# Optimization experiments

Hardware: AMD Instinct MI355X
Metric: run time of the kernel (lower is better)

Reference implementation:

```python
import jax, jax.numpy as jnp
import numpy as np

B = 1
NUM_STAGES = 3
HIDDEN_LENGTH = (512, 1024, 1536)
TOTAL = sum(HIDDEN_LENGTH)
ENC = 128
DIM = 1536
HEADS = 24
HEAD_DIM = 64
INNER = 4 * DIM
EPS = 1e-6
SCALE = HEAD_DIM ** -0.5


def _rope_freqs(S):
    # rotation-matrix RoPE table: [S, 1, D/2, 2, 2]
    pos = np.arange(S, dtype=np.float64)
    inv = 1.0 / (10000.0 ** (np.arange(0, HEAD_DIM, 2, dtype=np.float64) / HEAD_DIM))
    ang = pos[:, None] * inv[None, :]
    cos, sin = np.cos(ang), np.sin(ang)
    rot = np.stack([np.stack([cos, -sin], -1), np.stack([sin, cos], -1)], -2)
    return jnp.asarray(rot[:, None], dtype=jnp.float32)


def _layer_norm(x):
    m = x.mean(-1, keepdims=True)
    v = ((x - m) ** 2).mean(-1, keepdims=True)
    return (x - m) * jax.lax.rsqrt(v + EPS)


def _rms_norm(x, w):
    v = (x ** 2).mean(-1, keepdims=True)
    return x * jax.lax.rsqrt(v + EPS) * w


def _apply_rope(x, rot):
    # x: [B, S, H, D]; rot: [S, 1, D/2, 2, 2]
    xr = x.reshape(x.shape[:-1] + (HEAD_DIM // 2, 1, 2))
    out = rot[..., 0] * xr[..., 0] + rot[..., 1] * xr[..., 1]  # [B,S,H,D/2,2]
    return out.reshape(x.shape)


def _adaln_tokens(e6):
    # e6: [B*NUM_STAGES, 6*DIM] -> ragged per-token broadcast [B, TOTAL, 6*DIM]
    segs = [jnp.broadcast_to(e6[i::NUM_STAGES][:, None, :], (B, L, e6.shape[-1]))
            for i, L in enumerate(HIDDEN_LENGTH)]
    return jnp.concatenate(segs, axis=1)


def _ff(x, w1, b1, w2, b2):
    return jnp.dot(jax.nn.gelu(jnp.dot(x, w1) + b1, approximate=True), w2) + b2


def _forward(hidden_states, encoder_hidden_states, temb, enc_valid, rope_0, rope_1, rope_2,
             ada_w, ada_b, ada_ctx_w, ada_ctx_b,
             wq, bq, wk, bk, wv, bv, waq, baq, wak, bak, wav, bav,
             nq_w, nk_w, naq_w, nak_w, wo, bo, wao, bao,
             ff_w1, ff_b1, ff_w2, ff_b2, ffc_w1, ffc_b1, ffc_w2, ffc_b2):
    ropes = (rope_0, rope_1, rope_2)
    # AdaLN-Zero on hidden tokens (ragged per-stage modulation)
    tok = _adaln_tokens(jnp.dot(jax.nn.silu(temb), ada_w) + ada_b)
    shift_msa, scale_msa, gate_msa, shift_mlp, scale_mlp, gate_mlp = jnp.split(tok, 6, axis=2)
    nh = _layer_norm(hidden_states) * (1 + scale_msa) + shift_msa
    # AdaLN-Zero on context tokens
    ec = jnp.dot(jax.nn.silu(temb), ada_ctx_w) + ada_ctx_b
    c_shift, c_scale, c_gate, c_shift_mlp, c_scale_mlp, c_gate_mlp = jnp.split(ec, 6, axis=1)
    ne = _layer_norm(encoder_hidden_states) * (1 + c_scale[:, None]) + c_shift[:, None]

    # QKV projections + per-head RMSNorm on q/k
    q = _rms_norm((nh @ wq + bq).reshape(B, TOTAL, HEADS, HEAD_DIM), nq_w)
    k = _rms_norm((nh @ wk + bk).reshape(B, TOTAL, HEADS, HEAD_DIM), nk_w)
    v = (nh @ wv + bv).reshape(B, TOTAL, HEADS, HEAD_DIM)
    eq = _rms_norm((ne @ waq + baq).reshape(B * NUM_STAGES, ENC, HEADS, HEAD_DIM), naq_w)
    ek = _rms_norm((ne @ wak + bak).reshape(B * NUM_STAGES, ENC, HEADS, HEAD_DIM), nak_w)
    ev = (ne @ wav + bav).reshape(B * NUM_STAGES, ENC, HEADS, HEAD_DIM)

    hid_out, enc_out = [], []
    i_sum = 0
    for i, L in enumerate(HIDDEN_LENGTH):
        qi = _apply_rope(jnp.concatenate([eq[i::NUM_STAGES], q[:, i_sum:i_sum + L]], 1), ropes[i])
        ki = _apply_rope(jnp.concatenate([ek[i::NUM_STAGES], k[:, i_sum:i_sum + L]], 1), ropes[i])
        vi = jnp.concatenate([ev[i::NUM_STAGES], v[:, i_sum:i_sum + L]], 1)
        # T5-style key mask: only first enc_valid[i,b] text tokens are valid keys
        key_ok = jnp.concatenate([jnp.arange(ENC)[None, :] < enc_valid[i][:, None],
                                  jnp.ones((B, L), bool)], 1)  # [B, ENC+L]
        s = jnp.einsum('bqhd,bkhd->bhqk', qi, ki) * SCALE
        s = jnp.where(key_ok[:, None, None, :], s, jnp.finfo(s.dtype).min)
        o = jnp.einsum('bhqk,bkhd->bqhd', jax.nn.softmax(s, -1), vi).reshape(B, ENC + L, DIM)
        enc_out.append(o[:, :ENC])
        hid_out.append(o[:, ENC:])
        i_sum += L
    attn_h = jnp.concatenate(hid_out, 1) @ wo + bo
    attn_e = jnp.stack(enc_out, 1).reshape(B * NUM_STAGES, ENC, DIM) @ wao + bao

    # gated residuals + FFN
    h = hidden_states + gate_msa * attn_h
    h = h + gate_mlp * _ff(_layer_norm(h) * (1 + scale_mlp) + shift_mlp, ff_w1, ff_b1, ff_w2, ff_b2)
    e = encoder_hidden_states + c_gate[:, None] * attn_e
    e = e + c_gate_mlp[:, None] * _ff(_layer_norm(e) * (1 + c_scale_mlp[:, None]) + c_shift_mlp[:, None],
                                      ffc_w1, ffc_b1, ffc_w2, ffc_b2)
    return e, h


def setup_inputs() -> dict:
    ks = iter(jax.random.split(jax.random.key(0), 48))

    def nrm(shape, s):
        return jax.random.normal(next(ks), shape, jnp.float32) * s

    Z = lambda *shape: jnp.zeros(shape, jnp.float32)
    O = lambda *shape: jnp.ones(shape, jnp.float32)
    inp = {
        'hidden_states': nrm((B, TOTAL, DIM), 1.0),
        'encoder_hidden_states': nrm((B * NUM_STAGES, ENC, DIM), 1.0),
        'temb': nrm((B * NUM_STAGES, DIM), 1.0),
        'enc_valid': jax.random.randint(next(ks), (NUM_STAGES, B), 64, ENC + 1),
        'rope_0': _rope_freqs(ENC + HIDDEN_LENGTH[0]),
        'rope_1': _rope_freqs(ENC + HIDDEN_LENGTH[1]),
        'rope_2': _rope_freqs(ENC + HIDDEN_LENGTH[2]),
        'ada_w': nrm((DIM, 6 * DIM), 0.02), 'ada_b': nrm((6 * DIM,), 0.02),
        'ada_ctx_w': nrm((DIM, 6 * DIM), 0.02), 'ada_ctx_b': nrm((6 * DIM,), 0.02),
        'wq': nrm((DIM, DIM), 0.02), 'bq': Z(DIM),
        'wk': nrm((DIM, DIM), 0.02), 'bk': Z(DIM),
        'wv': nrm((DIM, DIM), 0.02), 'bv': Z(DIM),
        'waq': nrm((DIM, DIM), 0.02), 'baq': Z(DIM),
        'wak': nrm((DIM, DIM), 0.02), 'bak': Z(DIM),
        'wav': nrm((DIM, DIM), 0.02), 'bav': Z(DIM),
        'nq_w': O(HEAD_DIM), 'nk_w': O(HEAD_DIM), 'naq_w': O(HEAD_DIM), 'nak_w': O(HEAD_DIM),
        'wo': nrm((DIM, DIM), 0.02), 'bo': Z(DIM),
        'wao': nrm((DIM, DIM), 0.02), 'bao': Z(DIM),
        'ff_w1': nrm((DIM, INNER), 0.02), 'ff_b1': Z(INNER),
        'ff_w2': nrm((INNER, DIM), 0.02), 'ff_b2': Z(DIM),
        'ffc_w1': nrm((DIM, INNER), 0.02), 'ffc_b1': Z(INNER),
        'ffc_w2': nrm((INNER, DIM), 0.02), 'ffc_b2': Z(DIM),
    }
    return inp


def reference(hidden_states, encoder_hidden_states, temb, enc_valid, rope_0, rope_1, rope_2,
              ada_w, ada_b, ada_ctx_w, ada_ctx_b,
              wq, bq, wk, bk, wv, bv, waq, baq, wak, bak, wav, bav,
              nq_w, nk_w, naq_w, nak_w, wo, bo, wao, bao,
              ff_w1, ff_b1, ff_w2, ff_b2, ffc_w1, ffc_b1, ffc_w2, ffc_b2):
    return _forward(hidden_states, encoder_hidden_states, temb, enc_valid, rope_0, rope_1, rope_2,
                    ada_w, ada_b, ada_ctx_w, ada_ctx_b,
                    wq, bq, wk, bk, wv, bv, waq, baq, wak, bak, wav, bav,
                    nq_w, nk_w, naq_w, nak_w, wo, bo, wao, bao,
                    ff_w1, ff_b1, ff_w2, ff_b2, ffc_w1, ffc_b1, ffc_w2, ffc_b2)
```

## Files before the change

### kernel.cpp

```cpp
#include <hip/hip_runtime.h>
#include <hip/hip_bf16.h>

typedef __hip_bfloat16 bf16;
typedef short s16x8 __attribute__((ext_vector_type(8)));
typedef float f32x4 __attribute__((ext_vector_type(4)));

#define DIM   1536
#define HEADS 24
#define HD    64
#define TOTAL 3072
#define ENCR  384
#define INNER 6144
#define SIX   9216

__device__ __forceinline__ float ldf(const void* p, size_t i, int f) {
    return f ? ((const float*)p)[i]
             : __bfloat162float(((const bf16*)p)[i]);
}
__device__ __forceinline__ short f2s(float v) {
    bf16 b = __float2bfloat16(v);
    short s; __builtin_memcpy(&s, &b, 2); return s;
}
__device__ __forceinline__ s16x8 ldb8(const void* B, size_t i, int f) {
    s16x8 r;
    if (f) {
        const float4* p = (const float4*)((const float*)B + i);
        float4 x = p[0], y = p[1];
        r[0]=f2s(x.x); r[1]=f2s(x.y); r[2]=f2s(x.z); r[3]=f2s(x.w);
        r[4]=f2s(y.x); r[5]=f2s(y.y); r[6]=f2s(y.z); r[7]=f2s(y.w);
    } else {
        r = *(const s16x8*)((const short*)B + i);
    }
    return r;
}
__device__ __forceinline__ void gld16(const void* g, void* l) {
    __builtin_amdgcn_global_load_lds(
        (const __attribute__((address_space(1))) unsigned int*)g,
        (__attribute__((address_space(3))) unsigned int*)l, 16, 0, 0);
}

__global__ __launch_bounds__(256) void probe_kernel(const unsigned short* __restrict__ w,
                                                    int* __restrict__ flag) {
    __shared__ int cnt;
    if (threadIdx.x == 0) cnt = 0;
    __syncthreads();
    int local = 0;
    for (int i = threadIdx.x; i < 65536; i += 256) {
        unsigned short u = w[i];
        if (((u >> 7) & 0xFF) == 0xFF) local++;
    }
    atomicAdd(&cnt, local);
    __syncthreads();
    if (threadIdx.x == 0) flag[0] = (cnt > 0) ? 1 : 0;
}

__global__ __launch_bounds__(256) void silu_kernel(const void* __restrict__ temb,
                                                   float* __restrict__ sact,
                                                   const int* __restrict__ flag) {
    int f = flag[0];
    int i = blockIdx.x * 256 + threadIdx.x;
    float x = ldf(temb, i, f);
    sact[i] = x / (1.f + __expf(-x));
}

__global__ __launch_bounds__(256) void ada_kernel(const float* __restrict__ sact,
                                                  const void* __restrict__ W1,
                                                  const void* __restrict__ b1,
                                                  float* __restrict__ o1,
                                                  const void* __restrict__ W2,
                                                  const void* __restrict__ b2,
                                                  float* __restrict__ o2,
                                                  const int* __restrict__ flag) {
    int f = flag[0];
    __shared__ float red[3][4][64];
    int bx = blockIdx.x;
    const void* W; const void* bias; float* out;
    if (bx < 144) { W = W1; bias = b1; out = o1; }
    else          { W = W2; bias = b2; out = o2; bx -= 144; }
    int c   = threadIdx.x & 63;
    int col = bx * 64 + c;
    int kq  = threadIdx.x >> 6;
    float a0 = 0.f, a1 = 0.f, a2 = 0.f;
    for (int k = kq * 384; k < kq * 384 + 384; ++k) {
        float wv = ldf(W, (size_t)k * SIX + col, f);
        a0 += sact[k] * wv;
        a1 += sact[1536 + k] * wv;
        a2 += sact[3072 + k] * wv;
    }
    red[0][kq][c] = a0; red[1][kq][c] = a1; red[2][kq][c] = a2;
    __syncthreads();
    if (kq < 3) {
        float s = red[kq][0][c] + red[kq][1][c] + red[kq][2][c] + red[kq][3][c]
                + ldf(bias, col, f);
        out[(size_t)kq * SIX + col] = s;
    }
}

__global__ __launch_bounds__(256) void ln_mod_kernel(const void* __restrict__ xh,
                                                     const void* __restrict__ xe,
                                                     const float* __restrict__ adaH,
                                                     const float* __restrict__ adaE,
                                                     bf16* __restrict__ outh,
                                                     bf16* __restrict__ oute,
                                                     const int* __restrict__ flag) {
    int f = flag[0];
    __shared__ float r1[256], r2[256];
    int t = blockIdx.x, tid = threadIdx.x;
    const void* x; bf16* out; const float* ada; int stage;
    if (t < TOTAL) { x = xh; out = outh; ada = adaH; stage = t < 512 ? 0 : (t < 1536 ? 1 : 2); }
    else           { t -= TOTAL; x = xe; out = oute; ada = adaE; stage = t >> 7; }
    float v[6]; float s = 0.f, s2 = 0.f;
#pragma unroll
    for (int i = 0; i < 6; ++i) {
        float a = ldf(x, (size_t)t * DIM + tid + i * 256, f);
        v[i] = a; s += a; s2 += a * a;
    }
    r1[tid] = s; r2[tid] = s2;
    __syncthreads();
    for (int st = 128; st; st >>= 1) {
        if (tid < st) { r1[tid] += r1[tid + st]; r2[tid] += r2[tid + st]; }
        __syncthreads();
    }
    float mean = r1[0] * (1.f / 1536.f);
    float var  = fmaxf(r2[0] * (1.f / 1536.f) - mean * mean, 0.f);
    float inv  = rsqrtf(var + 1e-6f);
    const float* ab = ada + (size_t)stage * SIX;
#pragma unroll
    for (int i = 0; i < 6; ++i) {
        int c = tid + i * 256;
        float sc = ab[1 * DIM + c];
        float sh = ab[0 * DIM + c];
        out[(size_t)t * DIM + c] = __float2bfloat16((v[i] - mean) * inv * (1.f + sc) + sh);
    }
}

__global__ __launch_bounds__(256) void resid_ln_kernel(const void* __restrict__ bh,
                                                       const bf16* __restrict__ dh,
                                                       const float* __restrict__ adaH,
                                                       bf16* __restrict__ resh,
                                                       bf16* __restrict__ outh,
                                                       const void* __restrict__ be,
                                                       const bf16* __restrict__ de,
                                                       const float* __restrict__ adaE,
                                                       bf16* __restrict__ rese,
                                                       bf16* __restrict__ oute,
                                                       const int* __restrict__ flag) {
    int f = flag[0];
    __shared__ float r1[256], r2[256];
    int t = blockIdx.x, tid = threadIdx.x;
    const void* base; const bf16* delta; const float* ada; bf16* res; bf16* out; int stage;
    if (t < TOTAL) { base = bh; delta = dh; ada = adaH; res = resh; out = outh;
                     stage = t < 512 ? 0 : (t < 1536 ? 1 : 2); }
    else           { t -= TOTAL; base = be; delta = de; ada = adaE; res = rese; out = oute;
                     stage = t >> 7; }
    const float* ab = ada + (size_t)stage * SIX;
    float v[6]; float s = 0.f, s2 = 0.f;
#pragma unroll
    for (int i = 0; i < 6; ++i) {
        int c = tid + i * 256;
        size_t gi = (size_t)t * DIM + c;
        float g = ab[2 * DIM + c];
        float a = ldf(base, gi, f) + g * __bfloat162float(delta[gi]);
        res[gi] = __float2bfloat16(a);
        v[i] = a; s += a; s2 += a * a;
    }
    r1[tid] = s; r2[tid] = s2;
    __syncthreads();
    for (int st = 128; st; st >>= 1) {
        if (tid < st) { r1[tid] += r1[tid + st]; r2[tid] += r2[tid + st]; }
        __syncthreads();
    }
    float mean = r1[0] * (1.f / 1536.f);
    float var  = fmaxf(r2[0] * (1.f / 1536.f) - mean * mean, 0.f);
    float inv  = rsqrtf(var + 1e-6f);
#pragma unroll
    for (int i = 0; i < 6; ++i) {
        int c = tid + i * 256;
        float sc = ab[4 * DIM + c];
        float sh = ab[3 * DIM + c];
        out[(size_t)t * DIM + c] = __float2bfloat16((v[i] - mean) * inv * (1.f + sc) + sh);
    }
}

__device__ __forceinline__ void wt_body(const void* W, bf16* WT, int K, int N, int f) {
    __shared__ short T[64][72];
    int n0 = blockIdx.x * 64, k0 = blockIdx.y * 64;
    int tid = threadIdx.x;
    int r = tid >> 2, c0 = (tid & 3) * 16;
#pragma unroll
    for (int i = 0; i < 16; ++i)
        T[r][c0 + i] = f2s(ldf(W, (size_t)(k0 + r) * N + n0 + c0 + i, f));
    __syncthreads();
    int n = tid >> 2, kc = (tid & 3) * 16;
    s16x8 o0, o1;
#pragma unroll
    for (int i = 0; i < 8; ++i) o0[i] = T[kc + i][n];
#pragma unroll
    for (int i = 0; i < 8; ++i) o1[i] = T[kc + 8 + i][n];
    short* orow = (short*)WT + (size_t)(n0 + n) * K + k0 + kc;
    *(s16x8*)orow = o0;
    *(s16x8*)(orow + 8) = o1;
}

__global__ __launch_bounds__(256) void wt8_kernel(const void* s0, const void* s1,
                                                  const void* s2, const void* s3,
                                                  const void* s4, const void* s5,
                                                  const void* s6, const void* s7,
                                                  bf16* d0, bf16* d1, bf16* d2, bf16* d3,
                                                  bf16* d4, bf16* d5, bf16* d6, bf16* d7,
                                                  const int* __restrict__ flag) {
    const void* W; bf16* WT;
    switch (blockIdx.z) {
        case 0: W = s0; WT = d0; break;  case 1: W = s1; WT = d1; break;
        case 2: W = s2; WT = d2; break;  case 3: W = s3; WT = d3; break;
        case 4: W = s4; WT = d4; break;  case 5: W = s5; WT = d5; break;
        case 6: W = s6; WT = d6; break;  default: W = s7; WT = d7; break;
    }
    wt_body(W, WT, DIM, DIM, flag[0]);
}

__global__ __launch_bounds__(256) void wt2_kernel(const void* s0, const void* s1,
                                                  bf16* d0, bf16* d1, int K, int N,
                                                  const int* __restrict__ flag) {
    const void* W = blockIdx.z ? s1 : s0;
    bf16* WT = blockIdx.z ? d1 : d0;
    wt_body(W, WT, K, N, flag[0]);
}

__global__ __launch_bounds__(256) void gemm_t_kernel(const short* __restrict__ Ah,
                                                     const short* __restrict__ Ae,
                                                     const short* __restrict__ Bth,
                                                     const short* __restrict__ Bte,
                                                     const void* Bh0, const void* Bh1, const void* Bh2,
                                                     const void* Be0, const void* Be1, const void* Be2,
                                                     bf16* Oh0, bf16* Oh1, bf16* Oh2,
                                                     bf16* Oe0, bf16* Oe1, bf16* Oe2,
                                                     int yh, int Nout, int K, int act,
                                                     const int* __restrict__ flag) {
    int f = flag[0];
    __shared__ __align__(16) short As0[128 * 32];
    __shared__ __align__(16) short As1[128 * 32];
    __shared__ __align__(16) short As2[128 * 32];
    __shared__ __align__(16) short Bs0[128 * 32];
    __shared__ __align__(16) short Bs1[128 * 32];
    __shared__ __align__(16) short Bs2[128 * 32];
    int tid = threadIdx.x;
    int lane = tid & 63, wid = tid >> 6;
    int wy = wid >> 1, wx = wid & 1;
    int lane15 = lane & 15, quad = lane >> 4;

    int gx = gridDim.x;
    int nwg = gx * gridDim.y;
    int orig = blockIdx.y * gx + blockIdx.x;
    int q = nwg >> 3, r = nwg & 7;
    int x8 = orig & 7, o8 = orig >> 3;
    int wg = (x8 < r) ? x8 * (q + 1) + o8 : r * (q + 1) + (x8 - r) * q + o8;
    int bx = wg % gx, by = wg / gx;

    const short* A; const short* Bt; int m0;
    const void *b0, *b1, *b2; bf16 *o0, *o1, *o2;
    if (by < yh) { A = Ah; Bt = Bth; m0 = by * 128;
                   b0 = Bh0; b1 = Bh1; b2 = Bh2; o0 = Oh0; o1 = Oh1; o2 = Oh2; }
    else         { A = Ae; Bt = Bte; m0 = (by - yh) * 128;
                   b0 = Be0; b1 = Be1; b2 = Be2; o0 = Oe0; o1 = Oe1; o2 = Oe2; }
    int n0 = bx * 128;
    int lr = lane >> 2, lc = lane & 3;

    f32x4 acc[4][4] = {};

    auto stage = [&](short* Ad, short* Bd, int k0) {
#pragma unroll
        for (int c = 0; c < 2; ++c) {
            int rb = wid * 32 + c * 16;
            int rr = rb + lr;
            int gc = (lc - (rr >> 1)) & 3;
            gld16(A  + (size_t)(m0 + rr) * K + k0 + gc * 8, Ad + rb * 32);
            gld16(Bt + (size_t)(n0 + rr) * K + k0 + gc * 8, Bd + rb * 32);
        }
    };
    auto compute = [&](const short* Ash, const short* Bsh) {
        s16x8 af[4], bfr[4];
#pragma unroll
        for (int i = 0; i < 4; ++i) {
            int ra = wy * 64 + i * 16 + lane15;
            af[i] = *(const s16x8*)&Ash[ra * 32 + ((quad + (ra >> 1)) & 3) * 8];
            int rb2 = wx * 64 + i * 16 + lane15;
            bfr[i] = *(const s16x8*)&Bsh[rb2 * 32 + ((quad + (rb2 >> 1)) & 3) * 8];
        }
#pragma unroll
        for (int im = 0; im < 4; ++im)
#pragma unroll
            for (int in = 0; in < 4; ++in)
                acc[im][in] = __builtin_amdgcn_mfma_f32_16x16x32_bf16(
                    af[im], bfr[in], acc[im][in], 0, 0, 0);
    };
    int nt = K >> 5;
    auto step = [&](const short* Ac, const short* Bc, short* An, short* Bn, int tt) {
        int nx = tt + 2;
        if (nx < nt) {
            stage(An, Bn, nx << 5);
            asm volatile("s_waitcnt vmcnt(8)" ::: "memory");
        } else if (tt + 1 < nt) {
            asm volatile("s_waitcnt vmcnt(4)" ::: "memory");
        } else {
            asm volatile("s_waitcnt vmcnt(0)" ::: "memory");
        }
        __builtin_amdgcn_s_barrier();
        compute(Ac, Bc);
        asm volatile("s_waitcnt lgkmcnt(0)" ::: "memory");
        __builtin_amdgcn_s_barrier();
    };

    stage(As0, Bs0, 0);
    stage(As1, Bs1, 32);
    for (int t = 0; t < nt; t += 3) {
        step(As0, Bs0, As2, Bs2, t);
        step(As1, Bs1, As0, Bs0, t + 1);
        step(As2, Bs2, As1, Bs1, t + 2);
    }

    int sel = n0 / Nout;
    int nb = n0 - sel * Nout;
    bf16* Cout = sel == 0 ? o0 : (sel == 1 ? o1 : o2);
    const void* bs = sel == 0 ? b0 : (sel == 1 ? b1 : b2);

#pragma unroll
    for (int in = 0; in < 4; ++in) {
        int gn = nb + wx * 64 + in * 16 + lane15;
        float bsv = ldf(bs, gn, f);
#pragma unroll
        for (int im = 0; im < 4; ++im) {
#pragma unroll
            for (int rr = 0; rr < 4; ++rr) {
                int gm = m0 + wy * 64 + im * 16 + quad * 4 + rr;
                float v = acc[im][in][rr] + bsv;
                if (act == 1) {
                    float u = 0.7978845608028654f * (v + 0.044715f * v * v * v);
                    float e = __expf(2.f * u);
                    v = 0.5f * v * (1.f + (1.f - 2.f / (e + 1.f)));
                }
                Cout[(size_t)gm * Nout + gn] = __float2bfloat16(v);
            }
        }
    }
}

#define LDK 48
__global__ __launch_bounds__(256) void gemm_kernel(const short* __restrict__ A,
                                                   const void* __restrict__ B,
                                                   const void* __restrict__ bias,
                                                   bf16* __restrict__ C,
                                                   int M, int N, int K, int act,
                                                   const int* __restrict__ flag) {
    int f = flag[0];
    __shared__ __align__(16) short As[128 * LDK];
    __shared__ __align__(16) short Bs[128 * LDK];
    int tid = threadIdx.x;
    int lane = tid & 63, wid = tid >> 6;
    int wy = wid >> 1, wx = wid & 1;
    int m16 = lane & 15, quad = lane >> 4;
    int m0 = blockIdx.y * 128, n0 = blockIdx.x * 128;
    int ar0 = tid >> 2;
    int ac  = (tid & 3) * 8;
    int br0 = tid >> 4;
    int bc  = (tid & 15) * 8;
    f32x4 acc[4][4] = {};
    for (int k0 = 0; k0 < K; k0 += 32) {
        s16x8 a0 = *(const s16x8*)(A + (size_t)(m0 + ar0) * K + k0 + ac);
        s16x8 a1 = *(const s16x8*)(A + (size_t)(m0 + ar0 + 64) * K + k0 + ac);
        s16x8 b0 = ldb8(B, (size_t)(k0 + br0) * N + n0 + bc, f);
        s16x8 b1 = ldb8(B, (size_t)(k0 + br0 + 16) * N + n0 + bc, f);
        __syncthreads();
        *(s16x8*)(&As[ar0 * LDK + ac]) = a0;
        *(s16x8*)(&As[(ar0 + 64) * LDK + ac]) = a1;
#pragma unroll
        for (int i = 0; i < 8; ++i) {
            Bs[(bc + i) * LDK + br0] = b0[i];
            Bs[(bc + i) * LDK + br0 + 16] = b1[i];
        }
        __syncthreads();
        s16x8 af[4], bfr[4];
#pragma unroll
        for (int i = 0; i < 4; ++i) {
            af[i]  = *(const s16x8*)(&As[(wy * 64 + i * 16 + m16) * LDK + quad * 8]);
            bfr[i] = *(const s16x8*)(&Bs[(wx * 64 + i * 16 + m16) * LDK + quad * 8]);
        }
#pragma unroll
        for (int im = 0; im < 4; ++im)
#pragma unroll
            for (int in = 0; in < 4; ++in)
                acc[im][in] = __builtin_amdgcn_mfma_f32_16x16x32_bf16(
                    af[im], bfr[in], acc[im][in], 0, 0, 0);
    }
#pragma unroll
    for (int in = 0; in < 4; ++in) {
        int gn = n0 + wx * 64 + in * 16 + m16;
        float bsv = ldf(bias, gn, f);
#pragma unroll
        for (int im = 0; im < 4; ++im) {
#pragma unroll
            for (int r = 0; r < 4; ++r) {
                int gm = m0 + wy * 64 + im * 16 + quad * 4 + r;
                float v = acc[im][in][r] + bsv;
                if (act == 1) {
                    float u = 0.7978845608028654f * (v + 0.044715f * v * v * v);
                    float e = __expf(2.f * u);
                    v = 0.5f * v * (1.f + (1.f - 2.f / (e + 1.f)));
                }
                C[(size_t)gm * N + gn] = __float2bfloat16(v);
            }
        }
    }
}

__global__ __launch_bounds__(256) void rmsrope_kernel(bf16* __restrict__ Qb,
                                                      bf16* __restrict__ Kb,
                                                      bf16* __restrict__ EQb,
                                                      bf16* __restrict__ EKb,
                                                      const void* __restrict__ nq,
                                                      const void* __restrict__ nk,
                                                      const void* __restrict__ naq,
                                                      const void* __restrict__ nak,
                                                      const void* __restrict__ r0,
                                                      const void* __restrict__ r1,
                                                      const void* __restrict__ r2,
                                                      const int* __restrict__ flag) {
    int f = flag[0];
    int bid = blockIdx.x;
    bf16* x; const void* w; int is_enc;
    if (bid < 9216)       { x = Qb;  w = nq;  is_enc = 0; }
    else if (bid < 18432) { x = Kb;  w = nk;  is_enc = 0; bid -= 9216; }
    else if (bid < 19584) { x = EQb; w = naq; is_enc = 1; bid -= 18432; }
    else                  { x = EKb; w = nak; is_enc = 1; bid -= 19584; }
    int grp = bid * 8 + (threadIdx.x >> 5);
    int l = threadIdx.x & 31;
    int t = grp / 24;
    size_t base = (size_t)grp * 64 + 2 * l;
    unsigned int u = *(const unsigned int*)((const short*)x + base);
    union { unsigned int ui; float fl; } a, b;
    a.ui = (u & 0xFFFFu) << 16;
    b.ui = u & 0xFFFF0000u;
    float x0 = a.fl, x1 = b.fl;
    float ss = x0 * x0 + x1 * x1;
#pragma unroll
    for (int off = 1; off < 32; off <<= 1) ss += __shfl_xor(ss, off);
    float inv = rsqrtf(ss * (1.f / 64.f) + 1e-6f);
    float xw0 = x0 * inv * ldf(w, 2 * l, f);
    float xw1 = x1 * inv * ldf(w, 2 * l + 1, f);
    int stage, pos;
    if (is_enc)        { stage = t >> 7; pos = t & 127; }
    else if (t < 512)  { stage = 0; pos = 128 + t; }
    else if (t < 1536) { stage = 1; pos = 128 + t - 512; }
    else               { stage = 2; pos = 128 + t - 1536; }
    const void* rt = stage == 0 ? r0 : (stage == 1 ? r1 : r2);
    size_t ro = ((size_t)pos * 32 + l) * 4;
    float c00 = ldf(rt, ro + 0, f);
    float c01 = ldf(rt, ro + 1, f);
    float c10 = ldf(rt, ro + 2, f);
    float c11 = ldf(rt, ro + 3, f);
    unsigned int q0 = (unsigned int)(unsigned short)f2s(c00 * xw0 + c01 * xw1);
    unsigned int q1 = (unsigned int)(unsigned short)f2s(c10 * xw0 + c11 * xw1);
    *(unsigned int*)((short*)x + base) = (q1 << 16) | q0;
}

__global__ __launch_bounds__(256) void vjt_kernel(const bf16* __restrict__ Vb,
                                                  const bf16* __restrict__ EVb,
                                                  bf16* __restrict__ VJt) {
    __shared__ short T[64][72];
    int b = blockIdx.x;
    int h = b % 24, jt = b / 24;
    int s, j0, S, hbase; size_t off;
    if (jt < 10)      { s = 0; j0 = jt * 64;        S = 640;  hbase = 0;    off = 0; }
    else if (jt < 28) { s = 1; j0 = (jt - 10) * 64; S = 1152; hbase = 512;  off = (size_t)24 * 64 * 640; }
    else              { s = 2; j0 = (jt - 28) * 64; S = 1664; hbase = 1536; off = (size_t)24 * 64 * (640 + 1152); }
    int tid = threadIdx.x;
    int tr = tid >> 2, tc = (tid & 3) * 16;
    int j = j0 + tr;
    const bf16* vr = (j < 128) ? EVb + ((size_t)(s * 128 + j) * DIM + h * HD)
                               : Vb + ((size_t)(hbase + j - 128) * DIM + h * HD);
    *(s16x8*)&T[tr][tc]     = *(const s16x8*)((const short*)vr + tc);
    *(s16x8*)&T[tr][tc + 8] = *(const s16x8*)((const short*)vr + tc + 8);
    __syncthreads();
    int d = tid >> 2, c0 = (tid & 3) * 16;
    s16x8 o0, o1;
#pragma unroll
    for (int i = 0; i < 8; ++i) o0[i] = T[c0 + i][d];
#pragma unroll
    for (int i = 0; i < 8; ++i) o1[i] = T[c0 + 8 + i][d];
    short* orow = (short*)VJt + off + (size_t)(h * HD + d) * S + j0 + c0;
    *(s16x8*)orow = o0;
    *(s16x8*)(orow + 8) = o1;
}

__global__ __launch_bounds__(256) void attn_mfma_kernel(const bf16* __restrict__ Qb,
                                                        const bf16* __restrict__ Kb,
                                                        const bf16* __restrict__ EQ,
                                                        const bf16* __restrict__ EK,
                                                        const bf16* __restrict__ VJt,
                                                        const int* __restrict__ encv,
                                                        bf16* __restrict__ AH,
                                                        bf16* __restrict__ AE) {
    __shared__ __align__(16) short Ks[64 * 72];
    __shared__ __align__(16) short Vt[64 * 72];
    __shared__ __align__(16) short Ps[4][16 * 72];
    int tid = threadIdx.x, wid = tid >> 6, lane = tid & 63;
    int lane15 = lane & 15, quad = lane >> 4;
    int b = (int)gridDim.x - 1 - (int)blockIdx.x;
    int h = b % 24, qt = b / 24;
    int s, qt0, S, hbase; size_t voff;
    if (qt < 10)      { s = 0; qt0 = qt;      S = 640;  hbase = 0;    voff = 0; }
    else if (qt < 28) { s = 1; qt0 = qt - 10; S = 1152; hbase = 512;  voff = (size_t)24 * 64 * 640; }
    else              { s = 2; qt0 = qt - 28; S = 1664; hbase = 1536; voff = (size_t)24 * 64 * (640 + 1152); }
    const short* vbase = (const short*)VJt + voff + (size_t)h * HD * S;
    int ev = encv[s];
    int qbase = qt0 * 64 + wid * 16;

    int q = qbase + lane15;
    const short* qrow = (q < 128)
        ? (const short*)EQ + ((size_t)(s * 128 + q) * DIM + h * HD)
        : (const short*)Qb + ((size_t)(hbase + q - 128) * DIM + h * HD);
    s16x8 qa[2];
#pragma unroll
    for (int k0 = 0; k0 < 2; ++k0) {
        s16x8 x = *(const s16x8*)(qrow + k0 * 32 + quad * 8);
#pragma unroll
        for (int i = 0; i < 8; ++i) {
            union { unsigned int u; float fl; } t;
            t.u = ((unsigned int)(unsigned short)x[i]) << 16;
            t.fl *= 0.125f;
            x[i] = (short)(t.u >> 16);
        }
        qa[k0] = x;
    }

    f32x4 o[4] = {};
    float mrun[4] = {-1e30f, -1e30f, -1e30f, -1e30f};
    float lrun[4] = {};

    int nkb = S >> 6;
    for (int kb = 0; kb < nkb; ++kb) {
        __syncthreads();
        {
            int kr = tid >> 2, kc = (tid & 3) * 16;
            int kg = kb * 64 + kr;
            const short* krow = (kg < 128)
                ? (const short*)EK + ((size_t)(s * 128 + kg) * DIM + h * HD)
                : (const short*)Kb + ((size_t)(hbase + kg - 128) * DIM + h * HD);
            *(s16x8*)&Ks[kr * 72 + kc]     = *(const s16x8*)(krow + kc);
            *(s16x8*)&Ks[kr * 72 + kc + 8] = *(const s16x8*)(krow + kc + 8);
        }
        {
            int vd = tid >> 2, vc = (tid & 3) * 16;
            const short* vrow = vbase + (size_t)vd * S + kb * 64 + vc;
            *(s16x8*)&Vt[vd * 72 + vc]     = *(const s16x8*)(vrow);
            *(s16x8*)&Vt[vd * 72 + vc + 8] = *(const s16x8*)(vrow + 8);
        }
        __syncthreads();

        f32x4 sacc[4];
        __builtin_amdgcn_s_setprio(1);
#pragma unroll
        for (int g = 0; g < 4; ++g) {
            s16x8 kf0 = *(const s16x8*)&Ks[(g * 16 + lane15) * 72 + quad * 8];
            s16x8 kf1 = *(const s16x8*)&Ks[(g * 16 + lane15) * 72 + 32 + quad * 8];
            f32x4 c = {};
            c = __builtin_amdgcn_mfma_f32_16x16x32_bf16(qa[0], kf0, c, 0, 0, 0);
            c = __builtin_amdgcn_mfma_f32_16x16x32_bf16(qa[1], kf1, c, 0, 0, 0);
            sacc[g] = c;
        }
        __builtin_amdgcn_s_setprio(0);
        if (kb == 1) {
#pragma unroll
            for (int g = 0; g < 4; ++g) {
                int keyg = 64 + g * 16 + lane15;
                if (keyg >= ev) {
#pragma unroll
                    for (int r = 0; r < 4; ++r) sacc[g][r] = -1e30f;
                }
            }
        }
        float mt[4], al[4], ps[4];
#pragma unroll
        for (int r = 0; r < 4; ++r)
            mt[r] = fmaxf(fmaxf(sacc[0][r], sacc[1][r]), fmaxf(sacc[2][r], sacc[3][r]));
#pragma unroll
        for (int off = 1; off < 16; off <<= 1)
#pragma unroll
            for (int r = 0; r < 4; ++r) mt[r] = fmaxf(mt[r], __shfl_xor(mt[r], off));
#pragma unroll
        for (int r = 0; r < 4; ++r) {
            float mn = fmaxf(mrun[r], mt[r]);
            al[r] = __expf(mrun[r] - mn);
            mrun[r] = mn;
        }
#pragma unroll
        for (int g = 0; g < 4; ++g)
#pragma unroll
            for (int r = 0; r < 4; ++r)
                sacc[g][r] = __expf(sacc[g][r] - mrun[r]);
#pragma unroll
        for (int r = 0; r < 4; ++r)
            ps[r] = (sacc[0][r] + sacc[1][r]) + (sacc[2][r] + sacc[3][r]);
#pragma unroll
        for (int off = 1; off < 16; off <<= 1)
#pragma unroll
            for (int r = 0; r < 4; ++r) ps[r] += __shfl_xor(ps[r], off);
#pragma unroll
        for (int r = 0; r < 4; ++r) lrun[r] = lrun[r] * al[r] + ps[r];
#pragma unroll
        for (int dc = 0; dc < 4; ++dc)
#pragma unroll
            for (int r = 0; r < 4; ++r) o[dc][r] *= al[r];
#pragma unroll
        for (int g = 0; g < 4; ++g)
#pragma unroll
            for (int r = 0; r < 4; ++r)
                Ps[wid][(quad * 4 + r) * 72 + g * 16 + lane15] = f2s(sacc[g][r]);
        s16x8 pa0 = *(const s16x8*)&Ps[wid][lane15 * 72 + quad * 8];
        s16x8 pa1 = *(const s16x8*)&Ps[wid][lane15 * 72 + 32 + quad * 8];
        __builtin_amdgcn_s_setprio(1);
#pragma unroll
        for (int dc = 0; dc < 4; ++dc) {
            s16x8 vf0 = *(const s16x8*)&Vt[(dc * 16 + lane15) * 72 + quad * 8];
            s16x8 vf1 = *(const s16x8*)&Vt[(dc * 16 + lane15) * 72 + 32 + quad * 8];
            o[dc] = __builtin_amdgcn_mfma_f32_16x16x32_bf16(pa0, vf0, o[dc], 0, 0, 0);
            o[dc] = __builtin_amdgcn_mfma_f32_16x16x32_bf16(pa1, vf1, o[dc], 0, 0, 0);
        }
        __builtin_amdgcn_s_setprio(0);
    }

    float invl[4];
#pragma unroll
    for (int r = 0; r < 4; ++r) invl[r] = 1.f / fmaxf(lrun[r], 1e-37f);
#pragma unroll
    for (int r = 0; r < 4; ++r) {
        int qr = qbase + quad * 4 + r;
        bf16* orow = (qr < 128)
            ? AE + ((size_t)(s * 128 + qr) * DIM + h * HD)
            : AH + ((size_t)(hbase + qr - 128) * DIM + h * HD);
#pragma unroll
        for (int dc = 0; dc < 4; ++dc)
            orow[dc * 16 + lane15] = __float2bfloat16(o[dc][r] * invl[r]);
    }
}

__global__ __launch_bounds__(256) void resid_out_kernel(const bf16* __restrict__ bh,
                                                        const bf16* __restrict__ dh,
                                                        const float* __restrict__ adaH,
                                                        const bf16* __restrict__ be,
                                                        const bf16* __restrict__ de,
                                                        const float* __restrict__ adaE,
                                                        void* __restrict__ out,
                                                        const int* __restrict__ flag) {
    int ofl = flag[0];
    int bid = blockIdx.x, tid = threadIdx.x;
    float v; size_t oidx;
    if (bid < 2304) {
        int gid = bid * 256 + tid;
        int t = gid / DIM, c = gid - t * DIM;
        int st = t >> 7;
        v = __bfloat162float(be[gid]) + adaE[(size_t)st * SIX + 5 * DIM + c] * __bfloat162float(de[gid]);
        oidx = gid;
    } else {
        int gid = (bid - 2304) * 256 + tid;
        int t = gid / DIM, c = gid - t * DIM;
        int st = t < 512 ? 0 : (t < 1536 ? 1 : 2);
        v = __bfloat162float(bh[gid]) + adaH[(size_t)st * SIX + 5 * DIM + c] * __bfloat162float(dh[gid]);
        oidx = (size_t)ENCR * DIM + gid;
    }
    if (ofl) ((float*)out)[oidx] = v;
    else     ((bf16*)out)[oidx] = __float2bfloat16(v);
}

extern "C" void kernel_launch(void* const* d_in, const int* in_sizes, int n_in,
                              void* d_out, int out_size, void* d_ws, size_t ws_size,
                              hipStream_t stream) {
    (void)in_sizes; (void)n_in; (void)out_size;
    const void* hid   = d_in[0];
    const void* enc   = d_in[1];
    const void* temb  = d_in[2];
    const int*  encv  = (const int*)d_in[3];
    const void* rope0 = d_in[4];
    const void* rope1 = d_in[5];
    const void* rope2 = d_in[6];
    const void* ada_w = d_in[7];  const void* ada_b = d_in[8];
    const void* ada_cw = d_in[9]; const void* ada_cb = d_in[10];
    const void* wq = d_in[11]; const void* bq = d_in[12];
    const void* wk = d_in[13]; const void* bk = d_in[14];
    const void* wv = d_in[15]; const void* bv = d_in[16];
    const void* waq = d_in[17]; const void* baq = d_in[18];
    const void* wak = d_in[19]; const void* bak = d_in[20];
    const void* wav = d_in[21]; const void* bav = d_in[22];
    const void* nq_w = d_in[23];
    const void* nk_w = d_in[24];
    const void* naq_w = d_in[25];
    const void* nak_w = d_in[26];
    const void* wo = d_in[27]; const void* bo = d_in[28];
    const void* wao = d_in[29]; const void* bao = d_in[30];
    const void* ffw1 = d_in[31]; const void* ffb1 = d_in[32];
    const void* ffw2 = d_in[33]; const void* ffb2 = d_in[34];
    const void* fcw1 = d_in[35]; const void* fcb1 = d_in[36];
    const void* fcw2 = d_in[37]; const void* fcb2 = d_in[38];

    char* ws = (char*)d_ws;
    size_t off = 0;
    auto alloc = [&](size_t bytes) {
        char* p = ws + off;
        off = (off + bytes + 255) & ~(size_t)255;
        return p;
    };
    int*   FLAG = (int*)alloc(256);
    float* SACT = (float*)alloc(3 * 1536 * 4);
    float* E6   = (float*)alloc((size_t)3 * SIX * 4);
    float* EC   = (float*)alloc((size_t)3 * SIX * 4);
    bf16* NH  = (bf16*)alloc((size_t)TOTAL * DIM * 2);
    bf16* NE  = (bf16*)alloc((size_t)ENCR * DIM * 2);
    bf16* Qb  = (bf16*)alloc((size_t)TOTAL * DIM * 2);
    bf16* Kb  = (bf16*)alloc((size_t)TOTAL * DIM * 2);
    bf16* Vb  = (bf16*)alloc((size_t)TOTAL * DIM * 2);
    bf16* EQb = (bf16*)alloc((size_t)ENCR * DIM * 2);
    bf16* EKb = (bf16*)alloc((size_t)ENCR * DIM * 2);
    bf16* EVb = (bf16*)alloc((size_t)ENCR * DIM * 2);
    bf16* VJT = (bf16*)alloc((size_t)24 * 64 * (640 + 1152 + 1664) * 2);
    bf16* FF1  = (bf16*)alloc((size_t)TOTAL * INNER * 2);
    bf16* FFC1 = (bf16*)alloc((size_t)ENCR * INNER * 2);
    const size_t SQ = (size_t)DIM * DIM;
    const size_t RC = (size_t)DIM * INNER;
    bf16* WQKVT  = (bf16*)alloc(3 * SQ * 2);
    bf16* WAQKVT = (bf16*)alloc(3 * SQ * 2);
    bf16* WOT    = (bf16*)alloc(SQ * 2);
    bf16* WAOT   = (bf16*)alloc(SQ * 2);
    bf16* FFW1T  = (bf16*)alloc(RC * 2);
    bf16* FFW2T  = (bf16*)alloc(RC * 2);
    bf16* FCW1T  = (bf16*)alloc(RC * 2);
    bf16* FCW2T  = (bf16*)alloc(RC * 2);
    bool useT = (off <= ws_size);

    probe_kernel<<<1, 256, 0, stream>>>((const unsigned short*)ada_w, FLAG);

    if (useT) {
        wt8_kernel<<<dim3(24, 24, 8), 256, 0, stream>>>(
            wq, wk, wv, waq, wak, wav, wo, wao,
            WQKVT, WQKVT + SQ, WQKVT + 2 * SQ,
            WAQKVT, WAQKVT + SQ, WAQKVT + 2 * SQ,
            WOT, WAOT, FLAG);
        wt2_kernel<<<dim3(96, 24, 2), 256, 0, stream>>>(ffw1, fcw1, FFW1T, FCW1T, DIM, INNER, FLAG);
        wt2_kernel<<<dim3(24, 96, 2), 256, 0, stream>>>(ffw2, fcw2, FFW2T, FCW2T, INNER, DIM, FLAG);
    }

    silu_kernel<<<18, 256, 0, stream>>>(temb, SACT, FLAG);
    ada_kernel<<<288, 256, 0, stream>>>(SACT, ada_w, ada_b, E6, ada_cw, ada_cb, EC, FLAG);

    ln_mod_kernel<<<TOTAL + ENCR, 256, 0, stream>>>(hid, enc, E6, EC, NH, NE, FLAG);

    if (useT) {
        gemm_t_kernel<<<dim3(36, 27), 256, 0, stream>>>(
            (const short*)NH, (const short*)NE, (const short*)WQKVT, (const short*)WAQKVT,
            bq, bk, bv, baq, bak, bav,
            Qb, Kb, Vb, EQb, EKb, EVb, 24, DIM, DIM, 0, FLAG);
    } else {
        dim3 gh(12, 24), ge(12, 3);
        gemm_kernel<<<gh, 256, 0, stream>>>((const short*)NH, wq, bq, Qb, TOTAL, DIM, DIM, 0, FLAG);
        gemm_kernel<<<gh, 256, 0, stream>>>((const short*)NH, wk, bk, Kb, TOTAL, DIM, DIM, 0, FLAG);
        gemm_kernel<<<gh, 256, 0, stream>>>((const short*)NH, wv, bv, Vb, TOTAL, DIM, DIM, 0, FLAG);
        gemm_kernel<<<ge, 256, 0, stream>>>((const short*)NE, waq, baq, EQb, ENCR, DIM, DIM, 0, FLAG);
        gemm_kernel<<<ge, 256, 0, stream>>>((const short*)NE, wak, bak, EKb, ENCR, DIM, DIM, 0, FLAG);
        gemm_kernel<<<ge, 256, 0, stream>>>((const short*)NE, wav, bav, EVb, ENCR, DIM, DIM, 0, FLAG);
    }

    rmsrope_kernel<<<20736, 256, 0, stream>>>(Qb, Kb, EQb, EKb,
                                              nq_w, nk_w, naq_w, nak_w,
                                              rope0, rope1, rope2, FLAG);

    vjt_kernel<<<1296, 256, 0, stream>>>(Vb, EVb, VJT);

    attn_mfma_kernel<<<1296, 256, 0, stream>>>(Qb, Kb, EQb, EKb, VJT, encv, NH, NE);

    if (useT) {
        gemm_t_kernel<<<dim3(12, 27), 256, 0, stream>>>(
            (const short*)NH, (const short*)NE, (const short*)WOT, (const short*)WAOT,
            bo, bo, bo, bao, bao, bao,
            Qb, Qb, Qb, EQb, EQb, EQb, 24, DIM, DIM, 0, FLAG);
    } else {
        dim3 gh(12, 24), ge(12, 3);
        gemm_kernel<<<gh, 256, 0, stream>>>((const short*)NH, wo, bo, Qb, TOTAL, DIM, DIM, 0, FLAG);
        gemm_kernel<<<ge, 256, 0, stream>>>((const short*)NE, wao, bao, EQb, ENCR, DIM, DIM, 0, FLAG);
    }

    resid_ln_kernel<<<TOTAL + ENCR, 256, 0, stream>>>(hid, Qb, E6, Kb, Vb,
                                                      enc, EQb, EC, EKb, EVb, FLAG);

    if (useT) {
        gemm_t_kernel<<<dim3(48, 27), 256, 0, stream>>>(
            (const short*)Vb, (const short*)EVb, (const short*)FFW1T, (const short*)FCW1T,
            ffb1, ffb1, ffb1, fcb1, fcb1, fcb1,
            FF1, FF1, FF1, FFC1, FFC1, FFC1, 24, INNER, DIM, 1, FLAG);
        gemm_t_kernel<<<dim3(12, 27), 256, 0, stream>>>(
            (const short*)FF1, (const short*)FFC1, (const short*)FFW2T, (const short*)FCW2T,
            ffb2, ffb2, ffb2, fcb2, fcb2, fcb2,
            NH, NH, NH, NE, NE, NE, 24, DIM, INNER, 0, FLAG);
    } else {
        dim3 gh(12, 24), ge(12, 3), gf1(48, 24), gf1e(48, 3);
        gemm_kernel<<<gf1, 256, 0, stream>>>((const short*)Vb, ffw1, ffb1, FF1, TOTAL, INNER, DIM, 1, FLAG);
        gemm_kernel<<<gf1e, 256, 0, stream>>>((const short*)EVb, fcw1, fcb1, FFC1, ENCR, INNER, DIM, 1, FLAG);
        gemm_kernel<<<gh, 256, 0, stream>>>((const short*)FF1, ffw2, ffb2, NH, TOTAL, DIM, INNER, 0, FLAG);
        gemm_kernel<<<ge, 256, 0, stream>>>((const short*)FFC1, fcw2, fcb2, NE, ENCR, DIM, INNER, 0, FLAG);
    }

    resid_out_kernel<<<20736, 256, 0, stream>>>(Kb, NH, E6, EKb, NE, EC, d_out, FLAG);
}
```

Before: 1.135 ms.

## Fuse prep kernels, vectorize transposes, deepen GEMM ring and merge rmsrope with V transpose

The weight-transpose, SiLU and AdaLN projection launches are merged into one prep_kernel. Each AdaLN block now recomputes the SiLU of temb into shared memory. The transpose body switches from scalar loads to 8-wide vector loads. The GEMM ring grows from three to four shared-memory buffers so the trailing lgkmcnt wait and second barrier per k-step can be dropped, at the cost of more LDS per block and possibly lower occupancy. The RMSNorm/RoPE kernel and the V-transpose kernel are merged into one launch to cut launch overhead and let the two workloads overlap.

```diff
diff --git a/kernel.cpp b/kernel.cpp
--- a/kernel.cpp
+++ b/kernel.cpp
@@ -54,32 +54,81 @@
     if (threadIdx.x == 0) flag[0] = (cnt > 0) ? 1 : 0;
 }
 
-__global__ __launch_bounds__(256) void silu_kernel(const void* __restrict__ temb,
-                                                   float* __restrict__ sact,
-                                                   const int* __restrict__ flag) {
+__device__ __forceinline__ void wt_body(const void* W, bf16* WT, int K, int N,
+                                        int n0, int k0, int f) {
+    __shared__ short T[64][72];
+    int tid = threadIdx.x;
+    int r = tid >> 2, c0 = (tid & 3) * 16;
+    s16x8 v0 = ldb8(W, (size_t)(k0 + r) * N + n0 + c0, f);
+    s16x8 v1 = ldb8(W, (size_t)(k0 + r) * N + n0 + c0 + 8, f);
+    *(s16x8*)&T[r][c0] = v0;
+    *(s16x8*)&T[r][c0 + 8] = v1;
+    __syncthreads();
+    int n = tid >> 2, kc = (tid & 3) * 16;
+    s16x8 o0, o1;
+#pragma unroll
+    for (int i = 0; i < 8; ++i) o0[i] = T[kc + i][n];
+#pragma unroll
+    for (int i = 0; i < 8; ++i) o1[i] = T[kc + 8 + i][n];
+    short* orow = (short*)WT + (size_t)(n0 + n) * K + k0 + kc;
+    *(s16x8*)orow = o0;
+    *(s16x8*)(orow + 8) = o1;
+}
+
+__global__ __launch_bounds__(256) void prep_kernel(
+        const void* wq, const void* wk, const void* wv,
+        const void* waq, const void* wak, const void* wav,
+        const void* wo, const void* wao,
+        bf16* dq0, bf16* dq1, bf16* dq2, bf16* dq3,
+        bf16* dq4, bf16* dq5, bf16* dq6, bf16* dq7,
+        const void* ffw1, const void* fcw1, bf16* FFW1T, bf16* FCW1T,
+        const void* ffw2, const void* fcw2, bf16* FFW2T, bf16* FCW2T,
+        const void* temb,
+        const void* adaW1, const void* adaB1, float* adaO1,
+        const void* adaW2, const void* adaB2, float* adaO2,
+        int do_wt, const int* __restrict__ flag) {
     int f = flag[0];
-    int i = blockIdx.x * 256 + threadIdx.x;
-    float x = ldf(temb, i, f);
-    sact[i] = x / (1.f + __expf(-x));
-}
-
-__global__ __launch_bounds__(256) void ada_kernel(const float* __restrict__ sact,
-                                                  const void* __restrict__ W1,
-                                                  const void* __restrict__ b1,
-                                                  float* __restrict__ o1,
-                                                  const void* __restrict__ W2,
-                                                  const void* __restrict__ b2,
-                                                  float* __restrict__ o2,
-                                                  const int* __restrict__ flag) {
-    int f = flag[0];
+    int bid = blockIdx.x;
+    if (bid < 13824) {
+        if (!do_wt) return;
+        if (bid < 4608) {
+            int m = bid / 576, w = bid % 576;
+            const void* W; bf16* WT;
+            switch (m) {
+                case 0: W = wq;  WT = dq0; break;  case 1: W = wk;  WT = dq1; break;
+                case 2: W = wv;  WT = dq2; break;  case 3: W = waq; WT = dq3; break;
+                case 4: W = wak; WT = dq4; break;  case 5: W = wav; WT = dq5; break;
+                case 6: W = wo;  WT = dq6; break;  default: W = wao; WT = dq7; break;
+            }
+            wt_body(W, WT, DIM, DIM, (w % 24) * 64, (w / 24) * 64, f);
+        } else if (bid < 9216) {
+            int r2 = bid - 4608;
+            int m = r2 / 2304, w = r2 % 2304;
+            wt_body(m ? fcw1 : ffw1, m ? FCW1T : FFW1T, DIM, INNER,
+                    (w % 96) * 64, (w / 96) * 64, f);
+        } else {
+            int r2 = bid - 9216;
+            int m = r2 / 2304, w = r2 % 2304;
+            wt_body(m ? fcw2 : ffw2, m ? FCW2T : FFW2T, INNER, DIM,
+                    (w % 24) * 64, (w / 24) * 64, f);
+        }
+        return;
+    }
+    __shared__ float sact[4608];
     __shared__ float red[3][4][64];
-    int bx = blockIdx.x;
+    int tid = threadIdx.x;
+    for (int i = tid; i < 4608; i += 256) {
+        float x = ldf(temb, i, f);
+        sact[i] = x / (1.f + __expf(-x));
+    }
+    __syncthreads();
+    int bx = bid - 13824;
     const void* W; const void* bias; float* out;
-    if (bx < 144) { W = W1; bias = b1; out = o1; }
-    else          { W = W2; bias = b2; out = o2; bx -= 144; }
-    int c   = threadIdx.x & 63;
+    if (bx < 144) { W = adaW1; bias = adaB1; out = adaO1; }
+    else          { W = adaW2; bias = adaB2; out = adaO2; bx -= 144; }
+    int c   = tid & 63;
     int col = bx * 64 + c;
-    int kq  = threadIdx.x >> 6;
+    int kq  = tid >> 6;
     float a0 = 0.f, a1 = 0.f, a2 = 0.f;
     for (int k = kq * 384; k < kq * 384 + 384; ++k) {
         float wv = ldf(W, (size_t)k * SIX + col, f);
@@ -182,51 +231,6 @@
     }
 }
 
-__device__ __forceinline__ void wt_body(const void* W, bf16* WT, int K, int N, int f) {
-    __shared__ short T[64][72];
-    int n0 = blockIdx.x * 64, k0 = blockIdx.y * 64;
-    int tid = threadIdx.x;
-    int r = tid >> 2, c0 = (tid & 3) * 16;
-#pragma unroll
-    for (int i = 0; i < 16; ++i)
-        T[r][c0 + i] = f2s(ldf(W, (size_t)(k0 + r) * N + n0 + c0 + i, f));
-    __syncthreads();
-    int n = tid >> 2, kc = (tid & 3) * 16;
-    s16x8 o0, o1;
-#pragma unroll
-    for (int i = 0; i < 8; ++i) o0[i] = T[kc + i][n];
-#pragma unroll
-    for (int i = 0; i < 8; ++i) o1[i] = T[kc + 8 + i][n];
-    short* orow = (short*)WT + (size_t)(n0 + n) * K + k0 + kc;
-    *(s16x8*)orow = o0;
-    *(s16x8*)(orow + 8) = o1;
-}
-
-__global__ __launch_bounds__(256) void wt8_kernel(const void* s0, const void* s1,
-                                                  const void* s2, const void* s3,
-                                                  const void* s4, const void* s5,
-                                                  const void* s6, const void* s7,
-                                                  bf16* d0, bf16* d1, bf16* d2, bf16* d3,
-                                                  bf16* d4, bf16* d5, bf16* d6, bf16* d7,
-                                                  const int* __restrict__ flag) {
-    const void* W; bf16* WT;
-    switch (blockIdx.z) {
-        case 0: W = s0; WT = d0; break;  case 1: W = s1; WT = d1; break;
-        case 2: W = s2; WT = d2; break;  case 3: W = s3; WT = d3; break;
-        case 4: W = s4; WT = d4; break;  case 5: W = s5; WT = d5; break;
-        case 6: W = s6; WT = d6; break;  default: W = s7; WT = d7; break;
-    }
-    wt_body(W, WT, DIM, DIM, flag[0]);
-}
-
-__global__ __launch_bounds__(256) void wt2_kernel(const void* s0, const void* s1,
-                                                  bf16* d0, bf16* d1, int K, int N,
-                                                  const int* __restrict__ flag) {
-    const void* W = blockIdx.z ? s1 : s0;
-    bf16* WT = blockIdx.z ? d1 : d0;
-    wt_body(W, WT, K, N, flag[0]);
-}
-
 __global__ __launch_bounds__(256) void gemm_t_kernel(const short* __restrict__ Ah,
                                                      const short* __restrict__ Ae,
                                                      const short* __restrict__ Bth,
@@ -241,9 +245,11 @@
     __shared__ __align__(16) short As0[128 * 32];
     __shared__ __align__(16) short As1[128 * 32];
     __shared__ __align__(16) short As2[128 * 32];
+    __shared__ __align__(16) short As3[128 * 32];
     __shared__ __align__(16) short Bs0[128 * 32];
     __shared__ __align__(16) short Bs1[128 * 32];
     __shared__ __align__(16) short Bs2[128 * 32];
+    __shared__ __align__(16) short Bs3[128 * 32];
     int tid = threadIdx.x;
     int lane = tid & 63, wid = tid >> 6;
     int wy = wid >> 1, wx = wid & 1;
@@ -306,17 +312,17 @@
             asm volatile("s_waitcnt vmcnt(0)" ::: "memory");
         }
         __builtin_amdgcn_s_barrier();
+        __builtin_amdgcn_sched_barrier(0);
         compute(Ac, Bc);
-        asm volatile("s_waitcnt lgkmcnt(0)" ::: "memory");
-        __builtin_amdgcn_s_barrier();
     };
 
     stage(As0, Bs0, 0);
     stage(As1, Bs1, 32);
-    for (int t = 0; t < nt; t += 3) {
+    for (int t = 0; t < nt; t += 4) {
         step(As0, Bs0, As2, Bs2, t);
-        step(As1, Bs1, As0, Bs0, t + 1);
-        step(As2, Bs2, As1, Bs1, t + 2);
+        step(As1, Bs1, As3, Bs3, t + 1);
+        step(As2, Bs2, As0, Bs0, t + 2);
+        step(As3, Bs3, As1, Bs1, t + 3);
     }
 
     int sel = n0 / Nout;
@@ -413,20 +419,50 @@
     }
 }
 
-__global__ __launch_bounds__(256) void rmsrope_kernel(bf16* __restrict__ Qb,
-                                                      bf16* __restrict__ Kb,
-                                                      bf16* __restrict__ EQb,
-                                                      bf16* __restrict__ EKb,
-                                                      const void* __restrict__ nq,
-                                                      const void* __restrict__ nk,
-                                                      const void* __restrict__ naq,
-                                                      const void* __restrict__ nak,
-                                                      const void* __restrict__ r0,
-                                                      const void* __restrict__ r1,
-                                                      const void* __restrict__ r2,
-                                                      const int* __restrict__ flag) {
+__global__ __launch_bounds__(256) void rmsvjt_kernel(bf16* __restrict__ Qb,
+                                                     bf16* __restrict__ Kb,
+                                                     bf16* __restrict__ EQb,
+                                                     bf16* __restrict__ EKb,
+                                                     const void* __restrict__ nq,
+                                                     const void* __restrict__ nk,
+                                                     const void* __restrict__ naq,
+                                                     const void* __restrict__ nak,
+                                                     const void* __restrict__ r0,
+                                                     const void* __restrict__ r1,
+                                                     const void* __restrict__ r2,
+                                                     const bf16* __restrict__ Vb,
+                                                     const bf16* __restrict__ EVb,
+                                                     bf16* __restrict__ VJt,
+                                                     const int* __restrict__ flag) {
     int f = flag[0];
     int bid = blockIdx.x;
+    if (bid >= 20736) {
+        __shared__ short T[64][72];
+        int b = bid - 20736;
+        int h = b % 24, jt = b / 24;
+        int s, j0, S, hbase; size_t off;
+        if (jt < 10)      { s = 0; j0 = jt * 64;        S = 640;  hbase = 0;    off = 0; }
+        else if (jt < 28) { s = 1; j0 = (jt - 10) * 64; S = 1152; hbase = 512;  off = (size_t)24 * 64 * 640; }
+        else              { s = 2; j0 = (jt - 28) * 64; S = 1664; hbase = 1536; off = (size_t)24 * 64 * (640 + 1152); }
+        int tid = threadIdx.x;
+        int tr = tid >> 2, tc = (tid & 3) * 16;
+        int j = j0 + tr;
+        const bf16* vr = (j < 128) ? EVb + ((size_t)(s * 128 + j) * DIM + h * HD)
+                                   : Vb + ((size_t)(hbase + j - 128) * DIM + h * HD);
+        *(s16x8*)&T[tr][tc]     = *(const s16x8*)((const short*)vr + tc);
+        *(s16x8*)&T[tr][tc + 8] = *(const s16x8*)((const short*)vr + tc + 8);
+        __syncthreads();
+        int d = tid >> 2, c0 = (tid & 3) * 16;
+        s16x8 o0, o1;
+#pragma unroll
+        for (int i = 0; i < 8; ++i) o0[i] = T[c0 + i][d];
+#pragma unroll
+        for (int i = 0; i < 8; ++i) o1[i] = T[c0 + 8 + i][d];
+        short* orow = (short*)VJt + off + (size_t)(h * HD + d) * S + j0 + c0;
+        *(s16x8*)orow = o0;
+        *(s16x8*)(orow + 8) = o1;
+        return;
+    }
     bf16* x; const void* w; int is_enc;
     if (bid < 9216)       { x = Qb;  w = nq;  is_enc = 0; }
     else if (bid < 18432) { x = Kb;  w = nk;  is_enc = 0; bid -= 9216; }
@@ -437,10 +473,10 @@
     int t = grp / 24;
     size_t base = (size_t)grp * 64 + 2 * l;
     unsigned int u = *(const unsigned int*)((const short*)x + base);
-    union { unsigned int ui; float fl; } a, b;
+    union { unsigned int ui; float fl; } a, b2;
     a.ui = (u & 0xFFFFu) << 16;
-    b.ui = u & 0xFFFF0000u;
-    float x0 = a.fl, x1 = b.fl;
+    b2.ui = u & 0xFFFF0000u;
+    float x0 = a.fl, x1 = b2.fl;
     float ss = x0 * x0 + x1 * x1;
 #pragma unroll
     for (int off = 1; off < 32; off <<= 1) ss += __shfl_xor(ss, off);
@@ -461,35 +497,6 @@
     unsigned int q0 = (unsigned int)(unsigned short)f2s(c00 * xw0 + c01 * xw1);
     unsigned int q1 = (unsigned int)(unsigned short)f2s(c10 * xw0 + c11 * xw1);
     *(unsigned int*)((short*)x + base) = (q1 << 16) | q0;
-}
-
-__global__ __launch_bounds__(256) void vjt_kernel(const bf16* __restrict__ Vb,
-                                                  const bf16* __restrict__ EVb,
-                                                  bf16* __restrict__ VJt) {
-    __shared__ short T[64][72];
-    int b = blockIdx.x;
-    int h = b % 24, jt = b / 24;
-    int s, j0, S, hbase; size_t off;
-    if (jt < 10)      { s = 0; j0 = jt * 64;        S = 640;  hbase = 0;    off = 0; }
-    else if (jt < 28) { s = 1; j0 = (jt - 10) * 64; S = 1152; hbase = 512;  off = (size_t)24 * 64 * 640; }
-    else              { s = 2; j0 = (jt - 28) * 64; S = 1664; hbase = 1536; off = (size_t)24 * 64 * (640 + 1152); }
-    int tid = threadIdx.x;
-    int tr = tid >> 2, tc = (tid & 3) * 16;
-    int j = j0 + tr;
-    const bf16* vr = (j < 128) ? EVb + ((size_t)(s * 128 + j) * DIM + h * HD)
-                               : Vb + ((size_t)(hbase + j - 128) * DIM + h * HD);
-    *(s16x8*)&T[tr][tc]     = *(const s16x8*)((const short*)vr + tc);
-    *(s16x8*)&T[tr][tc + 8] = *(const s16x8*)((const short*)vr + tc + 8);
-    __syncthreads();
-    int d = tid >> 2, c0 = (tid & 3) * 16;
-    s16x8 o0, o1;
-#pragma unroll
-    for (int i = 0; i < 8; ++i) o0[i] = T[c0 + i][d];
-#pragma unroll
-    for (int i = 0; i < 8; ++i) o1[i] = T[c0 + 8 + i][d];
-    short* orow = (short*)VJt + off + (size_t)(h * HD + d) * S + j0 + c0;
-    *(s16x8*)orow = o0;
-    *(s16x8*)(orow + 8) = o1;
 }
 
 __global__ __launch_bounds__(256) void attn_mfma_kernel(const bf16* __restrict__ Qb,
@@ -710,7 +717,6 @@
         return p;
     };
     int*   FLAG = (int*)alloc(256);
-    float* SACT = (float*)alloc(3 * 1536 * 4);
     float* E6   = (float*)alloc((size_t)3 * SIX * 4);
     float* EC   = (float*)alloc((size_t)3 * SIX * 4);
     bf16* NH  = (bf16*)alloc((size_t)TOTAL * DIM * 2);
@@ -738,18 +744,14 @@
 
     probe_kernel<<<1, 256, 0, stream>>>((const unsigned short*)ada_w, FLAG);
 
-    if (useT) {
-        wt8_kernel<<<dim3(24, 24, 8), 256, 0, stream>>>(
-            wq, wk, wv, waq, wak, wav, wo, wao,
-            WQKVT, WQKVT + SQ, WQKVT + 2 * SQ,
-            WAQKVT, WAQKVT + SQ, WAQKVT + 2 * SQ,
-            WOT, WAOT, FLAG);
-        wt2_kernel<<<dim3(96, 24, 2), 256, 0, stream>>>(ffw1, fcw1, FFW1T, FCW1T, DIM, INNER, FLAG);
-        wt2_kernel<<<dim3(24, 96, 2), 256, 0, stream>>>(ffw2, fcw2, FFW2T, FCW2T, INNER, DIM, FLAG);
-    }
-
-    silu_kernel<<<18, 256, 0, stream>>>(temb, SACT, FLAG);
-    ada_kernel<<<288, 256, 0, stream>>>(SACT, ada_w, ada_b, E6, ada_cw, ada_cb, EC, FLAG);
+    prep_kernel<<<14112, 256, 0, stream>>>(
+        wq, wk, wv, waq, wak, wav, wo, wao,
+        WQKVT, WQKVT + SQ, WQKVT + 2 * SQ,
+        WAQKVT, WAQKVT + SQ, WAQKVT + 2 * SQ, WOT, WAOT,
+        ffw1, fcw1, FFW1T, FCW1T,
+        ffw2, fcw2, FFW2T, FCW2T,
+        temb, ada_w, ada_b, E6, ada_cw, ada_cb, EC,
+        useT ? 1 : 0, FLAG);
 
     ln_mod_kernel<<<TOTAL + ENCR, 256, 0, stream>>>(hid, enc, E6, EC, NH, NE, FLAG);
 
@@ -768,11 +770,10 @@
         gemm_kernel<<<ge, 256, 0, stream>>>((const short*)NE, wav, bav, EVb, ENCR, DIM, DIM, 0, FLAG);
     }
 
-    rmsrope_kernel<<<20736, 256, 0, stream>>>(Qb, Kb, EQb, EKb,
-                                              nq_w, nk_w, naq_w, nak_w,
-                                              rope0, rope1, rope2, FLAG);
-
-    vjt_kernel<<<1296, 256, 0, stream>>>(Vb, EVb, VJT);
+    rmsvjt_kernel<<<20736 + 1296, 256, 0, stream>>>(Qb, Kb, EQb, EKb,
+                                                    nq_w, nk_w, naq_w, nak_w,
+                                                    rope0, rope1, rope2,
+                                                    Vb, EVb, VJT, FLAG);
 
     attn_mfma_kernel<<<1296, 256, 0, stream>>>(Qb, Kb, EQb, EKb, VJT, encv, NH, NE);
 
```

Measured after the change: 1.026 ms. 9.7% less time.
